# Kernel tuning notes

Hardware: AMD Instinct MI355X
Metric: run time of the kernel (lower is better)

## Reference

```python
import jax, jax.numpy as jnp
import numpy as np

N = 200000   # total nodes across batched graphs
E = 3200000  # total edges
G = 1024     # number of graphs
MOL_DIM, HID, OUT = 9, 64, 64


def gcn_conv(x, W, b, src, dst, num_nodes):
    """PyG GCNConv: add self-loops, symmetric deg^{-1/2} normalization, linear first."""
    x = x @ W  # [N, H]
    loop = jnp.arange(num_nodes, dtype=src.dtype)
    s = jnp.concatenate([src, loop])
    d = jnp.concatenate([dst, loop])
    deg = jax.ops.segment_sum(jnp.ones_like(d, dtype=x.dtype), d, num_segments=num_nodes)
    dinv = jnp.where(deg > 0, jax.lax.rsqrt(deg), 0.0)
    norm = dinv[s] * dinv[d]                       # [E+N]
    msgs = x[s] * norm[:, None]                    # gather + scale
    out = jax.ops.segment_sum(msgs, d, num_segments=num_nodes)  # scatter-add
    return out + b


def setup_inputs() -> dict:
    key = jax.random.key(0)
    ks = jax.random.split(key, 12)
    def glorot(k, shp):
        scale = np.sqrt(2.0 / (shp[0] + shp[1])).astype(np.float32)
        return jax.random.normal(k, shp, dtype=jnp.float32) * scale
    return {
        "x": jax.random.normal(ks[0], (N, MOL_DIM), dtype=jnp.float32),
        "edge_index": jax.random.randint(ks[1], (2, E), 0, N, dtype=jnp.int32),
        "edge_attr": jax.random.normal(ks[2], (E, 3), dtype=jnp.float32),
        "batch": jnp.sort(jax.random.randint(ks[3], (N,), 0, G, dtype=jnp.int32)),
        "W1": glorot(ks[4], (MOL_DIM, HID)), "b1": jnp.zeros((HID,), jnp.float32),
        "W2": glorot(ks[5], (HID, HID)),     "b2": jnp.zeros((HID,), jnp.float32),
        "W3": glorot(ks[6], (HID, HID)),     "b3": jnp.zeros((HID,), jnp.float32),
        "Wl": glorot(ks[7], (2 * HID, OUT)), "bl": jnp.zeros((OUT,), jnp.float32),
    }


def reference(x, edge_index, edge_attr, batch, W1, b1, W2, b2, W3, b3, Wl, bl):
    src, dst = edge_index[0], edge_index[1]
    h = jax.nn.relu(gcn_conv(x, W1, b1, src, dst, N))
    h = jax.nn.relu(gcn_conv(h, W2, b2, src, dst, N))
    h = jax.nn.relu(gcn_conv(h, W3, b3, src, dst, N))
    # global mean/max pool over graphs
    counts = jax.ops.segment_sum(jnp.ones((N,), h.dtype), batch, num_segments=G)
    h_sum = jax.ops.segment_sum(h, batch, num_segments=G)
    h_mean = h_sum / jnp.maximum(counts, 1.0)[:, None]
    h_max = jax.ops.segment_max(h, batch, num_segments=G)
    pooled = jnp.concatenate([h_mean, h_max], axis=1)   # [G, 2H]
    return pooled @ Wl + bl
```

## Files before the change

kernel.cpp:

```cpp
#include <hip/hip_runtime.h>

typedef unsigned short u16;
typedef __attribute__((ext_vector_type(8))) short short8;
typedef __attribute__((ext_vector_type(4))) float float4v;

#define HID 64
#define MOLD 9
#define BSH 10
#define NBM 256
#define NBLK 256

__device__ __forceinline__ float bf2f(u16 u) {
    return __uint_as_float(((unsigned)u) << 16);
}
__device__ __forceinline__ u16 f2bf(float f) {
    unsigned x = __float_as_uint(f);
    unsigned r = (x + 0x7FFFu + ((x >> 16) & 1u)) >> 16;
    return (u16)r;
}
__device__ __forceinline__ void unpack_add(uint4 r, float* a) {
    a[0] += __uint_as_float(r.x << 16); a[1] += __uint_as_float(r.x & 0xffff0000u);
    a[2] += __uint_as_float(r.y << 16); a[3] += __uint_as_float(r.y & 0xffff0000u);
    a[4] += __uint_as_float(r.z << 16); a[5] += __uint_as_float(r.z & 0xffff0000u);
    a[6] += __uint_as_float(r.w << 16); a[7] += __uint_as_float(r.w & 0xffff0000u);
}
__device__ __forceinline__ void unpack_set(uint4 r, float* a) {
    a[0] = __uint_as_float(r.x << 16); a[1] = __uint_as_float(r.x & 0xffff0000u);
    a[2] = __uint_as_float(r.y << 16); a[3] = __uint_as_float(r.y & 0xffff0000u);
    a[4] = __uint_as_float(r.z << 16); a[5] = __uint_as_float(r.z & 0xffff0000u);
    a[6] = __uint_as_float(r.w << 16); a[7] = __uint_as_float(r.w & 0xffff0000u);
}

__global__ void k_detect(const u16* __restrict__ p, int n, int* __restrict__ flag) {
    bool bad = false;
    for (int i = threadIdx.x; i < n; i += 256) {
        float v = bf2f(p[i]);
        if (!(v == v) || fabsf(v) > 1000.f) bad = true;
    }
    if (bad) atomicOr(flag, 1);
}

__device__ __forceinline__ void cvt_seg(const void* src, u16* dst, int n, int mode) {
    if (mode) {
        const float* s = (const float*)src;
        for (int i = threadIdx.x; i < n; i += 256) dst[i] = f2bf(s[i]);
    } else {
        const u16* s = (const u16*)src;
        for (int i = threadIdx.x; i < n; i += 256) dst[i] = s[i];
    }
}

__global__ void k_cvt_w(const void* W1, const void* b1, const void* W2, const void* b2,
                        const void* W3, const void* b3, const void* Wl, const void* bl,
                        const int* __restrict__ flag, u16* __restrict__ wbf) {
    int mode = *flag;
    cvt_seg(W1, wbf + 0,     MOLD * HID, mode);
    cvt_seg(b1, wbf + 576,   HID, mode);
    cvt_seg(W2, wbf + 640,   HID * HID, mode);
    cvt_seg(b2, wbf + 4736,  HID, mode);
    cvt_seg(W3, wbf + 4800,  HID * HID, mode);
    cvt_seg(b3, wbf + 8896,  HID, mode);
    cvt_seg(Wl, wbf + 8960,  2 * HID * HID, mode);
    cvt_seg(bl, wbf + 17152, HID, mode);
}

__global__ void k_cvt_x(const void* __restrict__ src, u16* __restrict__ dst, int n,
                        const int* __restrict__ flag) {
    int mode = *flag;
    int i = blockIdx.x * 256 + threadIdx.x;
    if (i >= n) return;
    dst[i] = mode ? f2bf(((const float*)src)[i]) : ((const u16*)src)[i];
}

__global__ __launch_bounds__(256) void k_hist(const int* __restrict__ ei, int E, int nb,
                                              int chunk, int* __restrict__ cntmat) {
    __shared__ int h[NBM];
    int tid = threadIdx.x, k = blockIdx.x;
    for (int i = tid; i < nb; i += 256) h[i] = 0;
    __syncthreads();
    int e0 = k * chunk, e1 = e0 + chunk; if (e1 > E) e1 = E;
    for (int e = e0 + tid; e < e1; e += 256)
        atomicAdd(&h[ei[E + e] >> BSH], 1);
    __syncthreads();
    for (int b = tid; b < nb; b += 256) cntmat[b * NBLK + k] = h[b];
}

__global__ __launch_bounds__(1024) void k_scanmat(int* __restrict__ cntmat, int total) {
    __shared__ int ps[1024];
    int tid = threadIdx.x;
    int chunk = (total + 1023) >> 10;
    int i0 = tid * chunk, i1 = i0 + chunk; if (i1 > total) i1 = total;
    int sum = 0;
    for (int i = i0; i < i1; i++) sum += cntmat[i];
    ps[tid] = sum;
    __syncthreads();
    for (int off = 1; off < 1024; off <<= 1) {
        int t = (tid >= off) ? ps[tid - off] : 0;
        __syncthreads();
        ps[tid] += t;
        __syncthreads();
    }
    int run = ps[tid] - sum;
    for (int i = i0; i < i1; i++) { int c = cntmat[i]; cntmat[i] = run; run += c; }
}

__global__ __launch_bounds__(256) void k_scatter(const int* __restrict__ ei, int E, int nb,
                                                 int chunk, const int* __restrict__ offmat,
                                                 unsigned* __restrict__ staging) {
    __shared__ int cur[NBM];
    int tid = threadIdx.x, k = blockIdx.x;
    for (int b = tid; b < nb; b += 256) cur[b] = offmat[b * NBLK + k];
    __syncthreads();
    int e0 = k * chunk, e1 = e0 + chunk; if (e1 > E) e1 = E;
    for (int e = e0 + tid; e < e1; e += 256) {
        int s = ei[e];
        int d = ei[E + e];
        int b = d >> BSH;
        int p = atomicAdd(&cur[b], 1);
        staging[p] = (unsigned)s | ((unsigned)(d & ((1 << BSH) - 1)) << 18);
    }
}

__global__ __launch_bounds__(256) void k_p4(const unsigned* __restrict__ staging,
                                            const int* __restrict__ offmat, int nb, int N, int E,
                                            int* __restrict__ col, int* __restrict__ rowptr,
                                            float* __restrict__ dinv) {
    __shared__ int cnt[1 << BSH];
    __shared__ int cur[1 << BSH];
    __shared__ int ps[256];
    int b = blockIdx.x, tid = threadIdx.x;
    int s0 = offmat[b * NBLK];
    int s1 = (b == nb - 1) ? E : offmat[(b + 1) * NBLK];
    for (int i = tid; i < (1 << BSH); i += 256) cnt[i] = 0;
    __syncthreads();
    for (int i = s0 + tid; i < s1; i += 256)
        atomicAdd(&cnt[staging[i] >> 18], 1);
    __syncthreads();
    int base4 = tid * 4;
    int c0 = cnt[base4], c1 = cnt[base4 + 1], c2 = cnt[base4 + 2], c3 = cnt[base4 + 3];
    int tsum = c0 + c1 + c2 + c3;
    ps[tid] = tsum;
    __syncthreads();
    for (int off = 1; off < 256; off <<= 1) {
        int t = (tid >= off) ? ps[tid - off] : 0;
        __syncthreads();
        ps[tid] += t;
        __syncthreads();
    }
    int ex = ps[tid] - tsum;
    int o0 = s0 + ex, o1 = o0 + c0, o2 = o1 + c1, o3 = o2 + c2;
    cur[base4] = o0; cur[base4 + 1] = o1; cur[base4 + 2] = o2; cur[base4 + 3] = o3;
    int v = (b << BSH) + base4;
    if (v < N)     { rowptr[v] = o0;     dinv[v] = rsqrtf((float)(c0 + 1)); }
    if (v + 1 < N) { rowptr[v + 1] = o1; dinv[v + 1] = rsqrtf((float)(c1 + 1)); }
    if (v + 2 < N) { rowptr[v + 2] = o2; dinv[v + 2] = rsqrtf((float)(c2 + 1)); }
    if (v + 3 < N) { rowptr[v + 3] = o3; dinv[v + 3] = rsqrtf((float)(c3 + 1)); }
    if (b == nb - 1 && tid == 0) rowptr[N] = E;
    __syncthreads();
    for (int i = s0 + tid; i < s1; i += 256) {
        unsigned w = staging[i];
        int p = atomicAdd(&cur[w >> 18], 1);
        col[p] = (int)(w & 0x3FFFF);
    }
}

__global__ void k_l1(const u16* __restrict__ x, const u16* __restrict__ wseg,
                     const float* __restrict__ dinv, int N, u16* __restrict__ y) {
    __shared__ float w[MOLD * HID];
    int tid = threadIdx.x;
    for (int i = tid; i < MOLD * HID; i += blockDim.x) w[i] = bf2f(wseg[i]);
    __syncthreads();
    int v = blockIdx.x * 4 + (tid >> 6);
    int f = tid & 63;
    if (v >= N) return;
    float acc = 0.f;
#pragma unroll
    for (int k = 0; k < MOLD; k++) acc += bf2f(x[v * MOLD + k]) * w[k * HID + f];
    y[v * HID + f] = f2bf(dinv[v] * acc);
}

__device__ __forceinline__ void load_bias(const u16* bseg, int fg, float* breg) {
    uint4 bv = ((const uint4*)bseg)[fg];
    unpack_set(bv, breg);
}

__device__ __forceinline__ void gather_node(const u16* __restrict__ y,
                                            const int* __restrict__ rowptr,
                                            const int* __restrict__ col,
                                            float dv, const float* breg,
                                            int v, int eslot, int fg, float* hj) {
    float acc[8];
    const u16* yf = y + fg * 8;
    if (eslot == 0) {
        unpack_set(*(const uint4*)(yf + (size_t)v * HID), acc);
    } else {
#pragma unroll
        for (int j = 0; j < 8; j++) acc[j] = 0.f;
    }
    int s = rowptr[v], e = rowptr[v + 1];
    int i = s + eslot;
    for (; i + 8 < e; i += 16) {
        int u0 = col[i];
        int u1 = col[i + 8];
        uint4 r0 = *(const uint4*)(yf + (size_t)u0 * HID);
        uint4 r1 = *(const uint4*)(yf + (size_t)u1 * HID);
        unpack_add(r0, acc);
        unpack_add(r1, acc);
    }
    if (i < e) {
        int u = col[i];
        uint4 r = *(const uint4*)(yf + (size_t)u * HID);
        unpack_add(r, acc);
    }
#pragma unroll
    for (int j = 0; j < 8; j++) acc[j] += __shfl_xor(acc[j], 8);
#pragma unroll
    for (int j = 0; j < 8; j++) acc[j] += __shfl_xor(acc[j], 16);
#pragma unroll
    for (int j = 0; j < 8; j++) acc[j] += __shfl_xor(acc[j], 32);
#pragma unroll
    for (int j = 0; j < 8; j++) hj[j] = fmaxf(dv * acc[j] + breg[j], 0.f);
}

__device__ __forceinline__ void store_row(u16* __restrict__ h, int v, int fg, const float* hj) {
    uint4 o;
    o.x = (unsigned)f2bf(hj[0]) | ((unsigned)f2bf(hj[1]) << 16);
    o.y = (unsigned)f2bf(hj[2]) | ((unsigned)f2bf(hj[3]) << 16);
    o.z = (unsigned)f2bf(hj[4]) | ((unsigned)f2bf(hj[5]) << 16);
    o.w = (unsigned)f2bf(hj[6]) | ((unsigned)f2bf(hj[7]) << 16);
    ((uint4*)(h + (size_t)v * HID))[fg] = o;
}

__global__ __launch_bounds__(256, 4) void k_agg(
        const u16* __restrict__ y, const int* __restrict__ rowptr,
        const int* __restrict__ col, const float* __restrict__ dinv,
        const u16* __restrict__ bseg, int N, u16* __restrict__ h) {
    int lane = threadIdx.x & 63;
    int eslot = lane >> 3, fg = lane & 7;
    int wid = (blockIdx.x * blockDim.x + threadIdx.x) >> 6;
    int nw = (gridDim.x * blockDim.x) >> 6;
    float breg[8];
    load_bias(bseg, fg, breg);
    int cpw = (N + nw - 1) / nw;
    int v0 = wid * cpw;
    int v1 = v0 + cpw; if (v1 > N) v1 = N;
    for (int v = v0; v < v1; ++v) {
        float hj[8];
        gather_node(y, rowptr, col, dinv[v], breg, v, eslot, fg, hj);
        if (eslot == 0) store_row(h, v, fg, hj);
    }
}

__global__ __launch_bounds__(256, 4) void k_aggpool(
        const u16* __restrict__ y, const int* __restrict__ rowptr,
        const int* __restrict__ col, const float* __restrict__ dinv,
        const u16* __restrict__ bseg, const int* __restrict__ batch, int N,
        float* __restrict__ hsum, int* __restrict__ hmax, int* __restrict__ cnt) {
    int lane = threadIdx.x & 63;
    int eslot = lane >> 3, fg = lane & 7;
    int wid = (blockIdx.x * blockDim.x + threadIdx.x) >> 6;
    int nw = (gridDim.x * blockDim.x) >> 6;
    float breg[8];
    load_bias(bseg, fg, breg);
    int cpw = (N + nw - 1) / nw;
    int v0 = wid * cpw;
    int v1 = v0 + cpw; if (v1 > N) v1 = N;
    int gcur = -1, pcnt = 0;
    float psum[8], pmax[8];
#pragma unroll
    for (int j = 0; j < 8; j++) { psum[j] = 0.f; pmax[j] = 0.f; }
    for (int v = v0; v < v1; ++v) {
        float hj[8];
        gather_node(y, rowptr, col, dinv[v], breg, v, eslot, fg, hj);
        int g = batch[v];
        if (g != gcur) {
            if (gcur >= 0) {
                if (eslot == 0) {
#pragma unroll
                    for (int j = 0; j < 8; j++) {
                        atomicAdd(&hsum[gcur * HID + fg * 8 + j], psum[j]);
                        atomicMax(&hmax[gcur * HID + fg * 8 + j], __float_as_int(pmax[j]));
                    }
                }
                if (lane == 0) atomicAdd(&cnt[gcur], pcnt);
            }
#pragma unroll
            for (int j = 0; j < 8; j++) { psum[j] = 0.f; pmax[j] = 0.f; }
            pcnt = 0;
            gcur = g;
        }
        pcnt++;
#pragma unroll
        for (int j = 0; j < 8; j++) {
            psum[j] += hj[j];
            pmax[j] = fmaxf(pmax[j], hj[j]);
        }
    }
    if (gcur >= 0) {
        if (eslot == 0) {
#pragma unroll
            for (int j = 0; j < 8; j++) {
                atomicAdd(&hsum[gcur * HID + fg * 8 + j], psum[j]);
                atomicMax(&hmax[gcur * HID + fg * 8 + j], __float_as_int(pmax[j]));
            }
        }
        if (lane == 0) atomicAdd(&cnt[gcur], pcnt);
    }
}

__global__ __launch_bounds__(256, 4) void k_mm(
        const u16* __restrict__ h, const u16* __restrict__ W,
        const float* __restrict__ dinv, int N, u16* __restrict__ y) {
    int lane = threadIdx.x & 63;
    int q = lane >> 4, m = lane & 15;
    int wid = (blockIdx.x * blockDim.x + threadIdx.x) >> 6;
    int nw = (gridDim.x * blockDim.x) >> 6;
    short8 bfrag[4][2];
#pragma unroll
    for (int t = 0; t < 4; ++t)
#pragma unroll
        for (int kh = 0; kh < 2; ++kh) {
            short8 bv;
#pragma unroll
            for (int j = 0; j < 8; ++j)
                bv[j] = (short)W[(kh * 32 + q * 8 + j) * HID + t * 16 + m];
            bfrag[t][kh] = bv;
        }
    const float4v zero = {0.f, 0.f, 0.f, 0.f};
    int ntiles = (N + 15) >> 4;
    for (int tile = wid; tile < ntiles; tile += nw) {
        int base = tile * 16;
        int row = base + m;
        short8 a0 = {0, 0, 0, 0, 0, 0, 0, 0}, a1 = a0;
        if (row < N) {
            uint4 r0 = *(const uint4*)(h + (size_t)row * HID + q * 8);
            uint4 r1 = *(const uint4*)(h + (size_t)row * HID + 32 + q * 8);
            a0 = __builtin_bit_cast(short8, r0);
            a1 = __builtin_bit_cast(short8, r1);
        }
        float4v c[4];
#pragma unroll
        for (int t = 0; t < 4; ++t) c[t] = zero;
#pragma unroll
        for (int t = 0; t < 4; ++t) {
            c[t] = __builtin_amdgcn_mfma_f32_16x16x32_bf16(a0, bfrag[t][0], c[t], 0, 0, 0);
            c[t] = __builtin_amdgcn_mfma_f32_16x16x32_bf16(a1, bfrag[t][1], c[t], 0, 0, 0);
        }
#pragma unroll
        for (int r = 0; r < 4; ++r) {
            int node = base + q * 4 + r;
            if (node < N) {
                float dv = dinv[node];
#pragma unroll
                for (int t = 0; t < 4; ++t)
                    y[(size_t)node * HID + t * 16 + m] = f2bf(c[t][r] * dv);
            }
        }
    }
}

__global__ void k_final(const float* __restrict__ hsum, const int* __restrict__ hmaxi,
                        const int* __restrict__ cnt, const u16* __restrict__ wlseg,
                        const u16* __restrict__ blseg, const int* __restrict__ flag,
                        int G, void* __restrict__ out) {
    __shared__ float w[2 * HID * HID];
    int tid = threadIdx.x;
    for (int i = tid; i < 2 * HID * HID; i += blockDim.x) w[i] = bf2f(wlseg[i]);
    __syncthreads();
    int g = blockIdx.x * 4 + (tid >> 6);
    int f = tid & 63;
    if (g >= G) return;
    float inv = 1.f / fmaxf((float)cnt[g], 1.f);
    float acc = bf2f(blseg[f]);
#pragma unroll 8
    for (int k = 0; k < HID; k++) acc += (hsum[g * HID + k] * inv) * w[k * HID + f];
#pragma unroll 8
    for (int k = 0; k < HID; k++) acc += __int_as_float(hmaxi[g * HID + k]) * w[(HID + k) * HID + f];
    int mode = *flag;
    if (mode) ((float*)out)[g * HID + f] = acc;
    else      ((u16*)out)[g * HID + f] = f2bf(acc);
}

extern "C" void kernel_launch(void* const* d_in, const int* in_sizes, int n_in,
                              void* d_out, int out_size, void* d_ws, size_t ws_size,
                              hipStream_t stream) {
    const void* x  = d_in[0];
    const int*  ei = (const int*)d_in[1];
    const int*  batch = (const int*)d_in[3];

    const int NX = in_sizes[0];
    const int N  = NX / MOLD;
    const int E  = in_sizes[1] / 2;
    const int G  = out_size / HID;
    const int nb = (N + (1 << BSH) - 1) >> BSH;

    char* p = (char*)d_ws;
    auto alloc = [&](size_t bytes) -> char* {
        char* r = p;
        p += (bytes + 255) & ~(size_t)255;
        return r;
    };
    int*   flag    = (int*)alloc(256);
    int*   rowptr  = (int*)alloc((size_t)(N + 1) * 4);
    float* dinv    = (float*)alloc((size_t)N * 4);
    int*   cntmat  = (int*)alloc((size_t)nb * NBLK * 4);
    u16*   wbf     = (u16*)alloc((size_t)17216 * 2);
    int*   colb    = (int*)alloc((size_t)E * 4);
    size_t hb = (size_t)N * HID * 2;
    size_t sb = (size_t)E * 4;
    size_t xb = (size_t)NX * 2;
    size_t ub = hb > sb ? hb : sb; if (xb > ub) ub = xb;
    char* hbuf = alloc(ub);
    unsigned* staging = (unsigned*)hbuf;
    u16*      xbf     = (u16*)hbuf;
    u16*      hbf     = (u16*)hbuf;
    u16*   ybf  = (u16*)alloc((size_t)N * HID * 2);
    float* hsum = (float*)alloc((size_t)G * HID * 4);
    int*   hmax = (int*)alloc((size_t)G * HID * 4);
    int*   cnt  = (int*)alloc((size_t)G * 4);

    hipMemsetAsync(flag, 0, 256, stream);
    hipMemsetAsync(hsum, 0, (size_t)G * HID * 4, stream);
    hipMemsetAsync(hmax, 0, (size_t)G * HID * 4, stream);
    hipMemsetAsync(cnt, 0, (size_t)G * 4, stream);

    k_detect<<<1, 256, 0, stream>>>((const u16*)x, 8192, flag);
    k_cvt_w<<<1, 256, 0, stream>>>(d_in[4], d_in[5], d_in[6], d_in[7],
                                   d_in[8], d_in[9], d_in[10], d_in[11], flag, wbf);

    int chunk = (E + NBLK - 1) / NBLK;
    k_hist<<<NBLK, 256, 0, stream>>>(ei, E, nb, chunk, cntmat);
    k_scanmat<<<1, 1024, 0, stream>>>(cntmat, nb * NBLK);
    k_scatter<<<NBLK, 256, 0, stream>>>(ei, E, nb, chunk, cntmat, staging);
    k_p4<<<nb, 256, 0, stream>>>(staging, cntmat, nb, N, E, colb, rowptr, dinv);

    k_cvt_x<<<(NX + 255) / 256, 256, 0, stream>>>(x, xbf, NX, flag);
    k_l1<<<(N + 3) / 4, 256, 0, stream>>>(xbf, wbf + 0, dinv, N, ybf);

    k_agg<<<2048, 256, 0, stream>>>(ybf, rowptr, colb, dinv, wbf + 576, N, hbf);
    k_mm<<<1024, 256, 0, stream>>>(hbf, wbf + 640, dinv, N, ybf);
    k_agg<<<2048, 256, 0, stream>>>(ybf, rowptr, colb, dinv, wbf + 4736, N, hbf);
    k_mm<<<1024, 256, 0, stream>>>(hbf, wbf + 4800, dinv, N, ybf);
    k_aggpool<<<2048, 256, 0, stream>>>(ybf, rowptr, colb, dinv, wbf + 8896, batch, N,
                                        hsum, hmax, cnt);

    k_final<<<(G + 3) / 4, 256, 0, stream>>>(hsum, hmax, cnt, wbf + 8960, wbf + 17152,
                                             flag, G, d_out);
}
```

Before: 702.1 us.

## Use reduce-scatter shuffles so each lane owns one output feature

The cross-slot reduction no longer all-reduces eight values per lane with 24 shuffles. It now runs a reduce-scatter (8+4+2 shuffles), so each of the 64 lanes ends up holding one output feature. Stores, bias, pooling accumulators and atomics become per-lane scalars spread across all lanes instead of eight values on one eighth of the lanes. The edge loop loses its 2x unroll, which lowers memory-level parallelism. k_agg also moves from contiguous node chunks to a strided node assignment, which gives up locality within each wave.

```diff
diff --git a/kernel.cpp b/kernel.cpp
--- a/kernel.cpp
+++ b/kernel.cpp
@@ -179,16 +179,11 @@
     y[v * HID + f] = f2bf(dinv[v] * acc);
 }
 
-__device__ __forceinline__ void load_bias(const u16* bseg, int fg, float* breg) {
-    uint4 bv = ((const uint4*)bseg)[fg];
-    unpack_set(bv, breg);
-}
-
-__device__ __forceinline__ void gather_node(const u16* __restrict__ y,
-                                            const int* __restrict__ rowptr,
-                                            const int* __restrict__ col,
-                                            float dv, const float* breg,
-                                            int v, int eslot, int fg, float* hj) {
+__device__ __forceinline__ float gather_node_one(const u16* __restrict__ y,
+                                                 const int* __restrict__ rowptr,
+                                                 const int* __restrict__ col,
+                                                 float dv, float bias,
+                                                 int v, int eslot, int fg) {
     float acc[8];
     const u16* yf = y + fg * 8;
     if (eslot == 0) {
@@ -197,38 +192,28 @@
 #pragma unroll
         for (int j = 0; j < 8; j++) acc[j] = 0.f;
     }
-    int s = rowptr[v], e = rowptr[v + 1];
-    int i = s + eslot;
-    for (; i + 8 < e; i += 16) {
-        int u0 = col[i];
-        int u1 = col[i + 8];
-        uint4 r0 = *(const uint4*)(yf + (size_t)u0 * HID);
-        uint4 r1 = *(const uint4*)(yf + (size_t)u1 * HID);
-        unpack_add(r0, acc);
-        unpack_add(r1, acc);
-    }
-    if (i < e) {
+    int e = rowptr[v + 1];
+    for (int i = rowptr[v] + eslot; i < e; i += 8) {
         int u = col[i];
         uint4 r = *(const uint4*)(yf + (size_t)u * HID);
         unpack_add(r, acc);
     }
-#pragma unroll
-    for (int j = 0; j < 8; j++) acc[j] += __shfl_xor(acc[j], 8);
-#pragma unroll
-    for (int j = 0; j < 8; j++) acc[j] += __shfl_xor(acc[j], 16);
-#pragma unroll
-    for (int j = 0; j < 8; j++) acc[j] += __shfl_xor(acc[j], 32);
-#pragma unroll
-    for (int j = 0; j < 8; j++) hj[j] = fmaxf(dv * acc[j] + breg[j], 0.f);
-}
-
-__device__ __forceinline__ void store_row(u16* __restrict__ h, int v, int fg, const float* hj) {
-    uint4 o;
-    o.x = (unsigned)f2bf(hj[0]) | ((unsigned)f2bf(hj[1]) << 16);
-    o.y = (unsigned)f2bf(hj[2]) | ((unsigned)f2bf(hj[3]) << 16);
-    o.z = (unsigned)f2bf(hj[4]) | ((unsigned)f2bf(hj[5]) << 16);
-    o.w = (unsigned)f2bf(hj[6]) | ((unsigned)f2bf(hj[7]) << 16);
-    ((uint4*)(h + (size_t)v * HID))[fg] = o;
+    bool e0 = (eslot & 1) != 0, e1 = (eslot & 2) != 0, e2 = (eslot & 4) != 0;
+    float s[8];
+#pragma unroll
+    for (int j = 0; j < 8; j++) s[j] = acc[j] + __shfl_xor(acc[j], 8);
+    float b4[4];
+#pragma unroll
+    for (int k = 0; k < 4; k++) b4[k] = e0 ? s[k + 4] : s[k];
+#pragma unroll
+    for (int k = 0; k < 4; k++) b4[k] += __shfl_xor(b4[k], 16);
+    float c2[2];
+    c2[0] = e1 ? b4[2] : b4[0];
+    c2[1] = e1 ? b4[3] : b4[1];
+    c2[0] += __shfl_xor(c2[0], 32);
+    c2[1] += __shfl_xor(c2[1], 32);
+    float val = e2 ? c2[1] : c2[0];
+    return fmaxf(dv * val + bias, 0.f);
 }
 
 __global__ __launch_bounds__(256, 4) void k_agg(
@@ -237,17 +222,13 @@
         const u16* __restrict__ bseg, int N, u16* __restrict__ h) {
     int lane = threadIdx.x & 63;
     int eslot = lane >> 3, fg = lane & 7;
+    int idx = fg * 8 + ((eslot & 1) << 2) + (eslot & 2) + ((eslot >> 2) & 1);
+    float bias = bf2f(bseg[idx]);
     int wid = (blockIdx.x * blockDim.x + threadIdx.x) >> 6;
     int nw = (gridDim.x * blockDim.x) >> 6;
-    float breg[8];
-    load_bias(bseg, fg, breg);
-    int cpw = (N + nw - 1) / nw;
-    int v0 = wid * cpw;
-    int v1 = v0 + cpw; if (v1 > N) v1 = N;
-    for (int v = v0; v < v1; ++v) {
-        float hj[8];
-        gather_node(y, rowptr, col, dinv[v], breg, v, eslot, fg, hj);
-        if (eslot == 0) store_row(h, v, fg, hj);
+    for (int v = wid; v < N; v += nw) {
+        float hv = gather_node_one(y, rowptr, col, dinv[v], bias, v, eslot, fg);
+        h[(size_t)v * HID + idx] = f2bf(hv);
     }
 }
 
@@ -258,52 +239,34 @@
         float* __restrict__ hsum, int* __restrict__ hmax, int* __restrict__ cnt) {
     int lane = threadIdx.x & 63;
     int eslot = lane >> 3, fg = lane & 7;
+    int idx = fg * 8 + ((eslot & 1) << 2) + (eslot & 2) + ((eslot >> 2) & 1);
+    float bias = bf2f(bseg[idx]);
     int wid = (blockIdx.x * blockDim.x + threadIdx.x) >> 6;
     int nw = (gridDim.x * blockDim.x) >> 6;
-    float breg[8];
-    load_bias(bseg, fg, breg);
     int cpw = (N + nw - 1) / nw;
     int v0 = wid * cpw;
     int v1 = v0 + cpw; if (v1 > N) v1 = N;
     int gcur = -1, pcnt = 0;
-    float psum[8], pmax[8];
-#pragma unroll
-    for (int j = 0; j < 8; j++) { psum[j] = 0.f; pmax[j] = 0.f; }
+    float psum = 0.f, pmax = 0.f;
     for (int v = v0; v < v1; ++v) {
-        float hj[8];
-        gather_node(y, rowptr, col, dinv[v], breg, v, eslot, fg, hj);
+        float hv = gather_node_one(y, rowptr, col, dinv[v], bias, v, eslot, fg);
         int g = batch[v];
         if (g != gcur) {
             if (gcur >= 0) {
-                if (eslot == 0) {
-#pragma unroll
-                    for (int j = 0; j < 8; j++) {
-                        atomicAdd(&hsum[gcur * HID + fg * 8 + j], psum[j]);
-                        atomicMax(&hmax[gcur * HID + fg * 8 + j], __float_as_int(pmax[j]));
-                    }
-                }
+                atomicAdd(&hsum[gcur * HID + idx], psum);
+                atomicMax(&hmax[gcur * HID + idx], __float_as_int(pmax));
                 if (lane == 0) atomicAdd(&cnt[gcur], pcnt);
             }
-#pragma unroll
-            for (int j = 0; j < 8; j++) { psum[j] = 0.f; pmax[j] = 0.f; }
-            pcnt = 0;
+            psum = 0.f; pmax = 0.f; pcnt = 0;
             gcur = g;
         }
         pcnt++;
-#pragma unroll
-        for (int j = 0; j < 8; j++) {
-            psum[j] += hj[j];
-            pmax[j] = fmaxf(pmax[j], hj[j]);
-        }
+        psum += hv;
+        pmax = fmaxf(pmax, hv);
     }
     if (gcur >= 0) {
-        if (eslot == 0) {
-#pragma unroll
-            for (int j = 0; j < 8; j++) {
-                atomicAdd(&hsum[gcur * HID + fg * 8 + j], psum[j]);
-                atomicMax(&hmax[gcur * HID + fg * 8 + j], __float_as_int(pmax[j]));
-            }
-        }
+        atomicAdd(&hsum[gcur * HID + idx], psum);
+        atomicMax(&hmax[gcur * HID + idx], __float_as_int(pmax));
         if (lane == 0) atomicAdd(&cnt[gcur], pcnt);
     }
 }
```

Result: faster. 677.3 us (-3.5%).
